# Kernel optimization log

Measured on AMD Instinct MI355X. Metric: run time of the kernel, lower is better.

Reference implementation:

```python
import jax, jax.numpy as jnp
import numpy as np

B, L, NSTATE = 8192, 256, 9


def setup_inputs() -> dict:
    key = jax.random.key(0)
    k1, k2, k3, k4 = jax.random.split(key, 4)
    inputs = jax.random.normal(k1, (B, L, NSTATE), dtype=jnp.float32)
    path = jax.random.randint(k2, (B, L), 0, NSTATE, dtype=jnp.int32)
    # learned CRF params (init'd to zeros in the module; use small random for a
    # non-degenerate reference)
    tran = jax.random.normal(k3, (NSTATE, NSTATE), dtype=jnp.float32) * 0.1
    init = jax.random.normal(k4, (NSTATE,), dtype=jnp.float32) * 0.1
    return {"inputs": inputs, "path": path, "tran": tran, "init": init}


def reference(inputs, path, tran, init):
    # inputs: [B, L, S], path: [B, L], tran: [S, S], init: [S]
    # bio=False -> mask and imask are all zeros (no-op additions).
    # --- gold path score ---
    emit = jnp.take_along_axis(inputs, path[..., None], axis=-1)[..., 0]  # [B, L]
    tran_sc = tran[path[..., :-1], path[..., 1:]]                         # [B, L-1]
    path_scores = emit.sum(-1) + init[path[..., 0]] + tran_sc.sum(-1)     # [B]

    # --- partition function via log-semiring forward recurrence ---
    alpha0 = init + inputs[..., 0, :]                                     # [B, S]

    def step(alpha, x_t):
        # alpha: [B, S] (prev state), x_t: [B, S] (emission at t)
        nxt = alpha[..., :, None] + tran + x_t[..., None, :]              # [B, S, S]
        return jax.nn.logsumexp(nxt, axis=-2), None

    xs = jnp.moveaxis(inputs[..., 1:, :], -2, 0)                          # [L-1, B, S]
    alpha, _ = jax.lax.scan(step, alpha0, xs)
    scores = jax.nn.logsumexp(alpha, axis=-1)                             # [B]
    return scores - path_scores
```

## Files before the change

### kernel.cpp

```cpp
#include <hip/hip_runtime.h>


#define B_N 8192
#define L_N 256
#define S_N 9
#define SEQ_STRIDE 2304
#define HALF 128
#define SPB 6
#define XW 54
#define XSTRIDE 55
#define NBLK 22
#define PLS 129
#define NDIR_BLOCKS (B_N / 64)

#define LOG2E 1.44269504088896340736f
#define LN2f  0.69314718055994530942f

__device__ __forceinline__ void gl_lds4(const void* g, void* l) {
  __builtin_amdgcn_global_load_lds(
      (const __attribute__((address_space(1))) void*)g,
      (__attribute__((address_space(3))) void*)l, 4, 0, 0);
}

__device__ __forceinline__ float fexp(float x) {
  return __builtin_amdgcn_exp2f(x * LOG2E);
}

__global__ __launch_bounds__(64) void crf_half(
    const float* __restrict__ xg, const int* __restrict__ path,
    const float* __restrict__ tran, const float* __restrict__ initv,
    float* __restrict__ ws)
{
  __shared__ float lx[2][64 * XSTRIDE];
  __shared__ int   pl[64 * PLS];
  __shared__ float ltran[81];

  const int lane = threadIdx.x;
  const bool fwd = (int)blockIdx.x < NDIR_BLOCKS;
  const int seq0 = (fwd ? blockIdx.x : blockIdx.x - NDIR_BLOCKS) * 64;
  const int seq  = seq0 + lane;

  for (int i = lane; i < 81; i += 64) ltran[i] = tran[i];

  {
    const int t0 = fwd ? 0 : 127;
    const int* g = path + (size_t)seq0 * L_N + t0 + lane;
    for (int ss = 0; ss < 64; ++ss) {
      gl_lds4(g,      &pl[ss * PLS]);
      gl_lds4(g + 64, &pl[ss * PLS + 64]);
      g += L_N;
    }
    if (!fwd && lane == 0) {
      const int* g2 = path + (size_t)seq0 * L_N + 255;
      for (int ss = 0; ss < 64; ++ss) {
        gl_lds4(g2, &pl[ss * PLS + 128]);
        g2 += L_N;
      }
    }
  }

  if (lane < XW) {
    const int fbase = fwd ? 0 : (SEQ_STRIDE - XW);
    const float* g = xg + (size_t)seq0 * SEQ_STRIDE + fbase + lane;
    for (int ss = 0; ss < 64; ++ss) {
      gl_lds4(g, &lx[0][ss * XSTRIDE]);
      g += SEQ_STRIDE;
    }
  }

  float E[9][9];
#pragma unroll
  for (int a = 0; a < 9; ++a)
#pragma unroll
    for (int b = 0; b < 9; ++b)
      E[a][b] = fexp(fwd ? tran[b * 9 + a] : tran[a * 9 + b]);

  float st[9];
  float emit = 0.f, trn = 0.f;
  int ce = 0, pcur = 0;

  asm volatile("s_waitcnt vmcnt(0)" ::: "memory");

  if (!fwd) {
#pragma unroll
    for (int i = 0; i < 9; ++i) st[i] = 1.f;
    pcur = pl[lane * PLS + 128];
  }

  const int plbase = lane * PLS;
  const int xrow   = lane * XSTRIDE;

#pragma unroll 1
  for (int b = 0; b < NBLK; ++b) {
    asm volatile("s_waitcnt vmcnt(0)" ::: "memory");

    if (b + 1 < NBLK && lane < XW) {
      const int fb = fwd ? (b + 1) * XW : (SEQ_STRIDE - XW * (b + 2));
      const float* g = xg + (size_t)seq0 * SEQ_STRIDE + fb + lane;
      float* dst = &lx[(b + 1) & 1][0];
      for (int ss = 0; ss < 64; ++ss) {
        gl_lds4(g, dst + ss * XSTRIDE);
        g += SEQ_STRIDE;
      }
    }

    const float* lxb = &lx[b & 1][xrow];

    if (fwd) {
#pragma unroll
      for (int k = 0; k < SPB; ++k) {
        const int t = b * SPB + k;
        if (t >= HALF) break;
        const int off = k * 9;
        float xv[9];
#pragma unroll
        for (int j = 0; j < 9; ++j) xv[j] = lxb[off + j];
        if (t == 0) {
#pragma unroll
          for (int i = 0; i < 9; ++i) st[i] = fexp(initv[i] + xv[i]);
          pcur = pl[plbase];
          emit = lxb[off + pcur];
        } else {
          float e[9];
#pragma unroll
          for (int j = 0; j < 9; ++j) e[j] = fexp(xv[j]);
          float acc[9];
#pragma unroll
          for (int i = 0; i < 9; ++i) {
            float a = E[i][0] * st[0];
#pragma unroll
            for (int j = 1; j < 9; ++j) a = fmaf(E[i][j], st[j], a);
            acc[i] = a * e[i];
          }
#pragma unroll
          for (int i = 0; i < 9; ++i) st[i] = acc[i];
          const int p = pl[plbase + t];
          emit += lxb[off + p];
          trn  += ltran[pcur * 9 + p];
          pcur = p;
          if ((t & 7) == 7) {
            float m = st[0];
#pragma unroll
            for (int i = 1; i < 9; ++i) m = fmaxf(m, st[i]);
            const int ex = (int)((__float_as_uint(m) >> 23) & 0xffu) - 126;
            ce += ex;
            const float sc = __uint_as_float((unsigned)(127 - ex) << 23);
#pragma unroll
            for (int i = 0; i < 9; ++i) st[i] *= sc;
          }
        }
      }
    } else {
#pragma unroll
      for (int k = 0; k < SPB; ++k) {
        const int t = 255 - b * SPB - k;
        if (t < HALF) break;
        const int off = (SPB - 1 - k) * 9;
        float xv[9];
#pragma unroll
        for (int j = 0; j < 9; ++j) xv[j] = lxb[off + j];
        float w[9];
#pragma unroll
        for (int j = 0; j < 9; ++j) w[j] = fexp(xv[j]) * st[j];
        float acc[9];
#pragma unroll
        for (int i = 0; i < 9; ++i) {
          float a = E[i][0] * w[0];
#pragma unroll
          for (int j = 1; j < 9; ++j) a = fmaf(E[i][j], w[j], a);
          acc[i] = a;
        }
#pragma unroll
        for (int i = 0; i < 9; ++i) st[i] = acc[i];
        emit += lxb[off + pcur];
        const int pm = pl[plbase + (t - 1 - 127)];
        trn += ltran[pm * 9 + pcur];
        pcur = pm;
        if (((255 - t) & 7) == 7) {
          float m = st[0];
#pragma unroll
          for (int i = 1; i < 9; ++i) m = fmaxf(m, st[i]);
          const int ex = (int)((__float_as_uint(m) >> 23) & 0xffu) - 126;
          ce += ex;
          const float sc = __uint_as_float((unsigned)(127 - ex) << 23);
#pragma unroll
          for (int i = 0; i < 9; ++i) st[i] *= sc;
        }
      }
    }
  }

  float* wp = ws + seq;
  if (fwd) {
#pragma unroll
    for (int i = 0; i < 9; ++i) wp[i * B_N] = st[i];
    wp[9 * B_N] = (float)ce;
    const int p0 = pl[plbase];
    wp[10 * B_N] = emit + trn + initv[p0];
  } else {
#pragma unroll
    for (int i = 0; i < 9; ++i) wp[(11 + i) * B_N] = st[i];
    wp[20 * B_N] = (float)ce;
    wp[21 * B_N] = emit + trn;
  }
}

__global__ __launch_bounds__(256) void crf_combine(
    const float* __restrict__ ws, float* __restrict__ out)
{
  const int s = blockIdx.x * 256 + threadIdx.x;
  float dot = 0.f;
#pragma unroll
  for (int i = 0; i < 9; ++i)
    dot = fmaf(ws[i * B_N + s], ws[(11 + i) * B_N + s], dot);
  const float score =
      (__builtin_amdgcn_logf(dot) + ws[9 * B_N + s] + ws[20 * B_N + s]) * LN2f;
  out[s] = score - (ws[10 * B_N + s] + ws[21 * B_N + s]);
}

extern "C" void kernel_launch(void* const* d_in, const int* in_sizes, int n_in,
                              void* d_out, int out_size, void* d_ws, size_t ws_size,
                              hipStream_t stream) {
  (void)in_sizes; (void)n_in; (void)out_size; (void)ws_size;
  const float* xg    = (const float*)d_in[0];
  const int*   path  = (const int*)d_in[1];
  const float* tran  = (const float*)d_in[2];
  const float* initv = (const float*)d_in[3];
  float* ws  = (float*)d_ws;
  float* out = (float*)d_out;

  crf_half<<<2 * NDIR_BLOCKS, 64, 0, stream>>>(xg, path, tran, initv, ws);
  crf_combine<<<B_N / 256, 256, 0, stream>>>(ws, out);
}
```

Before: 153.0 us.

## Pack transition matvec into float2 FMAs and batch exps and renormalization per block

Reorganizes the exp-space transition matrix as float2 pairs so the 9x9 matvec can map to packed FMA instructions. All 54 emission exponentials of a block are computed up front, and the gold-path bookkeeping is split out of the recurrence loop. Renormalization moves from every 8 steps to once per 6-step block. This raises register pressure (54 exps, packed matrix), slightly increases renorm frequency, and relies on the compiler emitting v_pk_fma.

```diff
diff --git a/kernel.cpp b/kernel.cpp
--- a/kernel.cpp
+++ b/kernel.cpp
@@ -3,7 +3,6 @@
 
 #define B_N 8192
 #define L_N 256
-#define S_N 9
 #define SEQ_STRIDE 2304
 #define HALF 128
 #define SPB 6
@@ -16,6 +15,8 @@
 #define LOG2E 1.44269504088896340736f
 #define LN2f  0.69314718055994530942f
 
+typedef __attribute__((ext_vector_type(2))) float f32x2;
+
 __device__ __forceinline__ void gl_lds4(const void* g, void* l) {
   __builtin_amdgcn_global_load_lds(
       (const __attribute__((address_space(1))) void*)g,
@@ -68,12 +69,18 @@
     }
   }
 
-  float E[9][9];
-#pragma unroll
-  for (int a = 0; a < 9; ++a)
-#pragma unroll
-    for (int b = 0; b < 9; ++b)
-      E[a][b] = fexp(fwd ? tran[b * 9 + a] : tran[a * 9 + b]);
+  f32x2 EP[9][4];
+  float E8[9];
+#pragma unroll
+  for (int j = 0; j < 9; ++j) {
+#pragma unroll
+    for (int i2 = 0; i2 < 4; ++i2) {
+      float v0 = fexp(fwd ? tran[j * 9 + 2 * i2]     : tran[(2 * i2) * 9 + j]);
+      float v1 = fexp(fwd ? tran[j * 9 + 2 * i2 + 1] : tran[(2 * i2 + 1) * 9 + j]);
+      EP[j][i2] = (f32x2){v0, v1};
+    }
+    E8[j] = fexp(fwd ? tran[j * 9 + 8] : tran[8 * 9 + j]);
+  }
 
   float st[9];
   float emit = 0.f, trn = 0.f;
@@ -106,47 +113,53 @@
 
     const float* lxb = &lx[b & 1][xrow];
 
+    float e[XW];
+#pragma unroll
+    for (int q = 0; q < XW; ++q) e[q] = fexp(lxb[q]);
+
     if (fwd) {
+      int pv[SPB];
 #pragma unroll
       for (int k = 0; k < SPB; ++k) {
         const int t = b * SPB + k;
-        if (t >= HALF) break;
-        const int off = k * 9;
-        float xv[9];
-#pragma unroll
-        for (int j = 0; j < 9; ++j) xv[j] = lxb[off + j];
-        if (t == 0) {
-#pragma unroll
-          for (int i = 0; i < 9; ++i) st[i] = fexp(initv[i] + xv[i]);
-          pcur = pl[plbase];
-          emit = lxb[off + pcur];
-        } else {
-          float e[9];
-#pragma unroll
-          for (int j = 0; j < 9; ++j) e[j] = fexp(xv[j]);
-          float acc[9];
-#pragma unroll
-          for (int i = 0; i < 9; ++i) {
-            float a = E[i][0] * st[0];
-#pragma unroll
-            for (int j = 1; j < 9; ++j) a = fmaf(E[i][j], st[j], a);
-            acc[i] = a * e[i];
+        pv[k] = (t < HALF) ? pl[plbase + t] : 0;
+      }
+#pragma unroll
+      for (int k = 0; k < SPB; ++k) {
+        const int t = b * SPB + k;
+        if (t < HALF) {
+          if (t == 0) {
+            emit = lxb[pv[0]];
+          } else {
+            emit += lxb[k * 9 + pv[k]];
+            trn  += ltran[pcur * 9 + pv[k]];
           }
-#pragma unroll
-          for (int i = 0; i < 9; ++i) st[i] = acc[i];
-          const int p = pl[plbase + t];
-          emit += lxb[off + p];
-          trn  += ltran[pcur * 9 + p];
-          pcur = p;
-          if ((t & 7) == 7) {
-            float m = st[0];
-#pragma unroll
-            for (int i = 1; i < 9; ++i) m = fmaxf(m, st[i]);
-            const int ex = (int)((__float_as_uint(m) >> 23) & 0xffu) - 126;
-            ce += ex;
-            const float sc = __uint_as_float((unsigned)(127 - ex) << 23);
-#pragma unroll
-            for (int i = 0; i < 9; ++i) st[i] *= sc;
+          pcur = pv[k];
+        }
+      }
+#pragma unroll
+      for (int k = 0; k < SPB; ++k) {
+        const int t = b * SPB + k;
+        if (t < HALF) {
+          if (t == 0) {
+#pragma unroll
+            for (int i = 0; i < 9; ++i) st[i] = fexp(initv[i] + lxb[i]);
+          } else {
+            const int o = k * 9;
+            f32x2 a0 = EP[0][0] * st[0], a1 = EP[0][1] * st[0],
+                  a2 = EP[0][2] * st[0], a3 = EP[0][3] * st[0];
+            float a8 = E8[0] * st[0];
+#pragma unroll
+            for (int j = 1; j < 9; ++j) {
+              a0 += EP[j][0] * st[j]; a1 += EP[j][1] * st[j];
+              a2 += EP[j][2] * st[j]; a3 += EP[j][3] * st[j];
+              a8 = fmaf(E8[j], st[j], a8);
+            }
+            st[0] = a0.x * e[o + 0]; st[1] = a0.y * e[o + 1];
+            st[2] = a1.x * e[o + 2]; st[3] = a1.y * e[o + 3];
+            st[4] = a2.x * e[o + 4]; st[5] = a2.y * e[o + 5];
+            st[6] = a3.x * e[o + 6]; st[7] = a3.y * e[o + 7];
+            st[8] = a8 * e[o + 8];
           }
         }
       }
@@ -154,40 +167,46 @@
 #pragma unroll
       for (int k = 0; k < SPB; ++k) {
         const int t = 255 - b * SPB - k;
-        if (t < HALF) break;
-        const int off = (SPB - 1 - k) * 9;
-        float xv[9];
-#pragma unroll
-        for (int j = 0; j < 9; ++j) xv[j] = lxb[off + j];
-        float w[9];
-#pragma unroll
-        for (int j = 0; j < 9; ++j) w[j] = fexp(xv[j]) * st[j];
-        float acc[9];
-#pragma unroll
-        for (int i = 0; i < 9; ++i) {
-          float a = E[i][0] * w[0];
-#pragma unroll
-          for (int j = 1; j < 9; ++j) a = fmaf(E[i][j], w[j], a);
-          acc[i] = a;
-        }
-#pragma unroll
-        for (int i = 0; i < 9; ++i) st[i] = acc[i];
-        emit += lxb[off + pcur];
-        const int pm = pl[plbase + (t - 1 - 127)];
-        trn += ltran[pm * 9 + pcur];
-        pcur = pm;
-        if (((255 - t) & 7) == 7) {
-          float m = st[0];
-#pragma unroll
-          for (int i = 1; i < 9; ++i) m = fmaxf(m, st[i]);
-          const int ex = (int)((__float_as_uint(m) >> 23) & 0xffu) - 126;
-          ce += ex;
-          const float sc = __uint_as_float((unsigned)(127 - ex) << 23);
-#pragma unroll
-          for (int i = 0; i < 9; ++i) st[i] *= sc;
-        }
-      }
-    }
+        if (t >= HALF) {
+          const int o = (SPB - 1 - k) * 9;
+          emit += lxb[o + pcur];
+          const int pm = pl[plbase + (t - HALF)];
+          trn += ltran[pm * 9 + pcur];
+          pcur = pm;
+        }
+      }
+#pragma unroll
+      for (int k = 0; k < SPB; ++k) {
+        const int t = 255 - b * SPB - k;
+        if (t >= HALF) {
+          const int o = (SPB - 1 - k) * 9;
+          float w[9];
+#pragma unroll
+          for (int j = 0; j < 9; ++j) w[j] = e[o + j] * st[j];
+          f32x2 a0 = EP[0][0] * w[0], a1 = EP[0][1] * w[0],
+                a2 = EP[0][2] * w[0], a3 = EP[0][3] * w[0];
+          float a8 = E8[0] * w[0];
+#pragma unroll
+          for (int j = 1; j < 9; ++j) {
+            a0 += EP[j][0] * w[j]; a1 += EP[j][1] * w[j];
+            a2 += EP[j][2] * w[j]; a3 += EP[j][3] * w[j];
+            a8 = fmaf(E8[j], w[j], a8);
+          }
+          st[0] = a0.x; st[1] = a0.y; st[2] = a1.x; st[3] = a1.y;
+          st[4] = a2.x; st[5] = a2.y; st[6] = a3.x; st[7] = a3.y;
+          st[8] = a8;
+        }
+      }
+    }
+
+    float m = st[0];
+#pragma unroll
+    for (int i = 1; i < 9; ++i) m = fmaxf(m, st[i]);
+    const int ex = (int)((__float_as_uint(m) >> 23) & 0xffu) - 126;
+    ce += ex;
+    const float sc = __uint_as_float((unsigned)(127 - ex) << 23);
+#pragma unroll
+    for (int i = 0; i < 9; ++i) st[i] *= sc;
   }
 
   float* wp = ws + seq;
```

Result: faster. 147.5 us (-3.6%).

## Split each sequence's 9-state recurrence across 4 lanes using DPP rotations

Applied to the files above, without the earlier changes.

Each sequence is now handled by a quad of four lanes, each owning three states, so a wave covers 16 sequences instead of 64. Partner states are exchanged with DPP quad permutes, and the 9x9 transition matrix is held as rotated 3x3 blocks per lane. The grid grows fourfold, so more waves run in parallel and the serial chain per lane is shorter. The cost is padding waste (the fourth lane holds zeros), extra DPP moves per step, and renormalization that now runs once per block instead of every 8 steps.

```diff
diff --git a/kernel.cpp b/kernel.cpp
--- a/kernel.cpp
+++ b/kernel.cpp
@@ -3,7 +3,6 @@
 
 #define B_N 8192
 #define L_N 256
-#define S_N 9
 #define SEQ_STRIDE 2304
 #define HALF 128
 #define SPB 6
@@ -11,10 +10,17 @@
 #define XSTRIDE 55
 #define NBLK 22
 #define PLS 129
-#define NDIR_BLOCKS (B_N / 64)
+#define SPW 16
+#define NDIR_BLOCKS (B_N / SPW)
 
 #define LOG2E 1.44269504088896340736f
 #define LN2f  0.69314718055994530942f
+
+#define QP1 57
+#define QP2 78
+#define QP3 147
+#define QROT(src, CTRL) \
+  __int_as_float(__builtin_amdgcn_mov_dpp(__float_as_int(src), CTRL, 0xf, 0xf, 0))
 
 __device__ __forceinline__ void gl_lds4(const void* g, void* l) {
   __builtin_amdgcn_global_load_lds(
@@ -26,69 +32,70 @@
   return __builtin_amdgcn_exp2f(x * LOG2E);
 }
 
-__global__ __launch_bounds__(64) void crf_half(
+__global__ __launch_bounds__(64, 1) void crf_half(
     const float* __restrict__ xg, const int* __restrict__ path,
     const float* __restrict__ tran, const float* __restrict__ initv,
     float* __restrict__ ws)
 {
-  __shared__ float lx[2][64 * XSTRIDE];
-  __shared__ int   pl[64 * PLS];
+  __shared__ float lx[2][SPW * XSTRIDE];
+  __shared__ int   pl[SPW * PLS];
+  __shared__ int   pl255[SPW];
   __shared__ float ltran[81];
 
   const int lane = threadIdx.x;
+  const int c = lane & 3;
+  const int q = lane >> 2;
   const bool fwd = (int)blockIdx.x < NDIR_BLOCKS;
-  const int seq0 = (fwd ? blockIdx.x : blockIdx.x - NDIR_BLOCKS) * 64;
-  const int seq  = seq0 + lane;
+  const int seq0 = (fwd ? blockIdx.x : blockIdx.x - NDIR_BLOCKS) * SPW;
 
   for (int i = lane; i < 81; i += 64) ltran[i] = tran[i];
 
   {
     const int t0 = fwd ? 0 : 127;
-    const int* g = path + (size_t)seq0 * L_N + t0 + lane;
-    for (int ss = 0; ss < 64; ++ss) {
-      gl_lds4(g,      &pl[ss * PLS]);
-      gl_lds4(g + 64, &pl[ss * PLS + 64]);
-      g += L_N;
-    }
-    if (!fwd && lane == 0) {
-      const int* g2 = path + (size_t)seq0 * L_N + 255;
-      for (int ss = 0; ss < 64; ++ss) {
-        gl_lds4(g2, &pl[ss * PLS + 128]);
-        g2 += L_N;
+#pragma unroll
+    for (int r = 0; r < SPW; ++r) {
+      const int* g = path + (size_t)(seq0 + r) * L_N + t0 + lane;
+      gl_lds4(g,      &pl[r * PLS]);
+      gl_lds4(g + 64, &pl[r * PLS + 64]);
+    }
+  }
+  if (!fwd && lane < SPW)
+    pl255[lane] = path[(size_t)(seq0 + lane) * L_N + 255];
+
+  if (lane < XW) {
+    const int fb = fwd ? 0 : (SEQ_STRIDE - XW);
+#pragma unroll
+    for (int r = 0; r < SPW; ++r)
+      gl_lds4(xg + (size_t)(seq0 + r) * SEQ_STRIDE + fb + lane,
+              &lx[0][r * XSTRIDE]);
+  }
+
+  float Erot[4][3][3];
+#pragma unroll
+  for (int r = 0; r < 4; ++r)
+#pragma unroll
+    for (int k = 0; k < 3; ++k)
+#pragma unroll
+      for (int i = 0; i < 3; ++i) {
+        const int ig = 3 * c + i;
+        const int jg = 3 * ((c + r) & 3) + k;
+        float v = 0.f;
+        if (ig < 9 && jg < 9)
+          v = fexp(fwd ? tran[jg * 9 + ig] : tran[ig * 9 + jg]);
+        Erot[r][k][i] = v;
       }
-    }
-  }
-
-  if (lane < XW) {
-    const int fbase = fwd ? 0 : (SEQ_STRIDE - XW);
-    const float* g = xg + (size_t)seq0 * SEQ_STRIDE + fbase + lane;
-    for (int ss = 0; ss < 64; ++ss) {
-      gl_lds4(g, &lx[0][ss * XSTRIDE]);
-      g += SEQ_STRIDE;
-    }
-  }
-
-  float E[9][9];
-#pragma unroll
-  for (int a = 0; a < 9; ++a)
-#pragma unroll
-    for (int b = 0; b < 9; ++b)
-      E[a][b] = fexp(fwd ? tran[b * 9 + a] : tran[a * 9 + b]);
-
-  float st[9];
+
+  float o[3];
   float emit = 0.f, trn = 0.f;
   int ce = 0, pcur = 0;
 
-  asm volatile("s_waitcnt vmcnt(0)" ::: "memory");
-
   if (!fwd) {
 #pragma unroll
-    for (int i = 0; i < 9; ++i) st[i] = 1.f;
-    pcur = pl[lane * PLS + 128];
-  }
-
-  const int plbase = lane * PLS;
-  const int xrow   = lane * XSTRIDE;
+    for (int k = 0; k < 3; ++k) o[k] = (c < 3) ? 1.f : 0.f;
+    pcur = pl255[q];
+  }
+
+  const int myoff = (c == 3) ? 0 : 3 * c;
 
 #pragma unroll 1
   for (int b = 0; b < NBLK; ++b) {
@@ -96,112 +103,145 @@
 
     if (b + 1 < NBLK && lane < XW) {
       const int fb = fwd ? (b + 1) * XW : (SEQ_STRIDE - XW * (b + 2));
-      const float* g = xg + (size_t)seq0 * SEQ_STRIDE + fb + lane;
       float* dst = &lx[(b + 1) & 1][0];
-      for (int ss = 0; ss < 64; ++ss) {
-        gl_lds4(g, dst + ss * XSTRIDE);
-        g += SEQ_STRIDE;
+#pragma unroll
+      for (int r = 0; r < SPW; ++r)
+        gl_lds4(xg + (size_t)(seq0 + r) * SEQ_STRIDE + fb + lane,
+                dst + r * XSTRIDE);
+    }
+
+    const float* lxq = &lx[b & 1][q * XSTRIDE];
+
+    float e[SPB * 3];
+#pragma unroll
+    for (int tt = 0; tt < SPB; ++tt)
+#pragma unroll
+      for (int k = 0; k < 3; ++k)
+        e[tt * 3 + k] = fexp(lxq[tt * 9 + myoff + k]);
+
+    if (fwd) {
+#pragma unroll
+      for (int kk = 0; kk < SPB; ++kk) {
+        const int t = b * SPB + kk;
+        if (t < HALF) {
+          if (t == 0) {
+#pragma unroll
+            for (int k = 0; k < 3; ++k)
+              o[k] = (c < 3) ? fexp(initv[3 * c + k] + lxq[myoff + k]) : 0.f;
+            pcur = pl[q * PLS];
+            emit = lxq[pcur];
+          } else {
+            float g[4][3];
+#pragma unroll
+            for (int k = 0; k < 3; ++k) {
+              g[0][k] = o[k];
+              g[1][k] = QROT(o[k], QP1);
+              g[2][k] = QROT(o[k], QP2);
+              g[3][k] = QROT(o[k], QP3);
+            }
+            if (kk == 0 && b > 0) {
+              float m = g[0][0];
+#pragma unroll
+              for (int r = 0; r < 4; ++r)
+#pragma unroll
+                for (int k = 0; k < 3; ++k) m = fmaxf(m, g[r][k]);
+              const int ex = (int)((__float_as_uint(m) >> 23) & 0xffu) - 126;
+              ce += ex;
+              const float sc = __uint_as_float((unsigned)(127 - ex) << 23);
+#pragma unroll
+              for (int r = 0; r < 4; ++r)
+#pragma unroll
+                for (int k = 0; k < 3; ++k) g[r][k] *= sc;
+            }
+            float out[3];
+#pragma unroll
+            for (int i = 0; i < 3; ++i) {
+              float a = Erot[0][0][i] * g[0][0];
+#pragma unroll
+              for (int r = 0; r < 4; ++r)
+#pragma unroll
+                for (int k = 0; k < 3; ++k)
+                  if (r + k > 0) a = fmaf(Erot[r][k][i], g[r][k], a);
+              out[i] = a;
+            }
+            const int p = pl[q * PLS + t];
+            emit += lxq[kk * 9 + p];
+            trn  += ltran[pcur * 9 + p];
+            pcur = p;
+#pragma unroll
+            for (int i = 0; i < 3; ++i) o[i] = out[i] * e[kk * 3 + i];
+          }
+        }
       }
-    }
-
-    const float* lxb = &lx[b & 1][xrow];
-
-    if (fwd) {
-#pragma unroll
-      for (int k = 0; k < SPB; ++k) {
-        const int t = b * SPB + k;
-        if (t >= HALF) break;
-        const int off = k * 9;
-        float xv[9];
-#pragma unroll
-        for (int j = 0; j < 9; ++j) xv[j] = lxb[off + j];
-        if (t == 0) {
-#pragma unroll
-          for (int i = 0; i < 9; ++i) st[i] = fexp(initv[i] + xv[i]);
-          pcur = pl[plbase];
-          emit = lxb[off + pcur];
-        } else {
-          float e[9];
-#pragma unroll
-          for (int j = 0; j < 9; ++j) e[j] = fexp(xv[j]);
-          float acc[9];
-#pragma unroll
-          for (int i = 0; i < 9; ++i) {
-            float a = E[i][0] * st[0];
-#pragma unroll
-            for (int j = 1; j < 9; ++j) a = fmaf(E[i][j], st[j], a);
-            acc[i] = a * e[i];
-          }
-#pragma unroll
-          for (int i = 0; i < 9; ++i) st[i] = acc[i];
-          const int p = pl[plbase + t];
-          emit += lxb[off + p];
-          trn  += ltran[pcur * 9 + p];
-          pcur = p;
-          if ((t & 7) == 7) {
-            float m = st[0];
-#pragma unroll
-            for (int i = 1; i < 9; ++i) m = fmaxf(m, st[i]);
+    } else {
+#pragma unroll
+      for (int kk = 0; kk < SPB; ++kk) {
+        const int t = 255 - b * SPB - kk;
+        if (t >= HALF) {
+          const int tt = SPB - 1 - kk;
+          float w[3];
+#pragma unroll
+          for (int k = 0; k < 3; ++k) w[k] = e[tt * 3 + k] * o[k];
+          float g[4][3];
+#pragma unroll
+          for (int k = 0; k < 3; ++k) {
+            g[0][k] = w[k];
+            g[1][k] = QROT(w[k], QP1);
+            g[2][k] = QROT(w[k], QP2);
+            g[3][k] = QROT(w[k], QP3);
+          }
+          if (kk == 0 && b > 0) {
+            float m = g[0][0];
+#pragma unroll
+            for (int r = 0; r < 4; ++r)
+#pragma unroll
+              for (int k = 0; k < 3; ++k) m = fmaxf(m, g[r][k]);
             const int ex = (int)((__float_as_uint(m) >> 23) & 0xffu) - 126;
             ce += ex;
             const float sc = __uint_as_float((unsigned)(127 - ex) << 23);
 #pragma unroll
-            for (int i = 0; i < 9; ++i) st[i] *= sc;
-          }
+            for (int r = 0; r < 4; ++r)
+#pragma unroll
+              for (int k = 0; k < 3; ++k) g[r][k] *= sc;
+          }
+#pragma unroll
+          for (int i = 0; i < 3; ++i) {
+            float a = Erot[0][0][i] * g[0][0];
+#pragma unroll
+            for (int r = 0; r < 4; ++r)
+#pragma unroll
+              for (int k = 0; k < 3; ++k)
+                if (r + k > 0) a = fmaf(Erot[r][k][i], g[r][k], a);
+            o[i] = a;
+          }
+          emit += lxq[tt * 9 + pcur];
+          const int pm = pl[q * PLS + (t - 1 - 127)];
+          trn += ltran[pm * 9 + pcur];
+          pcur = pm;
         }
       }
+    }
+  }
+
+  const int sq = seq0 + q;
+  float* wp = ws + sq;
+  if (fwd) {
+    if (c < 3) {
+#pragma unroll
+      for (int k = 0; k < 3; ++k) wp[(3 * c + k) * B_N] = o[k];
     } else {
-#pragma unroll
-      for (int k = 0; k < SPB; ++k) {
-        const int t = 255 - b * SPB - k;
-        if (t < HALF) break;
-        const int off = (SPB - 1 - k) * 9;
-        float xv[9];
-#pragma unroll
-        for (int j = 0; j < 9; ++j) xv[j] = lxb[off + j];
-        float w[9];
-#pragma unroll
-        for (int j = 0; j < 9; ++j) w[j] = fexp(xv[j]) * st[j];
-        float acc[9];
-#pragma unroll
-        for (int i = 0; i < 9; ++i) {
-          float a = E[i][0] * w[0];
-#pragma unroll
-          for (int j = 1; j < 9; ++j) a = fmaf(E[i][j], w[j], a);
-          acc[i] = a;
-        }
-#pragma unroll
-        for (int i = 0; i < 9; ++i) st[i] = acc[i];
-        emit += lxb[off + pcur];
-        const int pm = pl[plbase + (t - 1 - 127)];
-        trn += ltran[pm * 9 + pcur];
-        pcur = pm;
-        if (((255 - t) & 7) == 7) {
-          float m = st[0];
-#pragma unroll
-          for (int i = 1; i < 9; ++i) m = fmaxf(m, st[i]);
-          const int ex = (int)((__float_as_uint(m) >> 23) & 0xffu) - 126;
-          ce += ex;
-          const float sc = __uint_as_float((unsigned)(127 - ex) << 23);
-#pragma unroll
-          for (int i = 0; i < 9; ++i) st[i] *= sc;
-        }
-      }
-    }
-  }
-
-  float* wp = ws + seq;
-  if (fwd) {
-#pragma unroll
-    for (int i = 0; i < 9; ++i) wp[i * B_N] = st[i];
-    wp[9 * B_N] = (float)ce;
-    const int p0 = pl[plbase];
-    wp[10 * B_N] = emit + trn + initv[p0];
+      wp[9 * B_N] = (float)ce;
+      const int p0 = pl[q * PLS];
+      wp[10 * B_N] = emit + trn + initv[p0];
+    }
   } else {
-#pragma unroll
-    for (int i = 0; i < 9; ++i) wp[(11 + i) * B_N] = st[i];
-    wp[20 * B_N] = (float)ce;
-    wp[21 * B_N] = emit + trn;
+    if (c < 3) {
+#pragma unroll
+      for (int k = 0; k < 3; ++k) wp[(11 + 3 * c + k) * B_N] = o[k];
+    } else {
+      wp[20 * B_N] = (float)ce;
+      wp[21 * B_N] = emit + trn;
+    }
   }
 }
 
```

After: 133.7 us. -12.6%, faster.
